# Kernel tuning notes

Hardware: AMD Instinct MI355X
Metric: run time of the kernel (lower is better)

## Reference

```python
import jax, jax.numpy as jnp
import numpy as np

D_MODEL = 2048
NUM_HEADS = 16
HEAD_DIM = D_MODEL // NUM_HEADS
B, T = 2, 2048


def setup_inputs() -> dict:
    key = jax.random.key(0)
    ks = jax.random.split(key, 6)
    x = jax.random.normal(ks[0], (B, T, D_MODEL), dtype=jnp.float32)
    # RoPE tables: angles theta_i = 10000^(-2i/d), half-dim tables [T, HEAD_DIM//2]
    pos = jnp.arange(T, dtype=jnp.float32)[:, None]
    inv_freq = 1.0 / (10000.0 ** (jnp.arange(0, HEAD_DIM, 2, dtype=jnp.float32) / HEAD_DIM))
    ang = pos * inv_freq[None, :]
    sin = jnp.sin(ang)
    cos = jnp.cos(ang)
    doc_ids = jnp.sort(jax.random.randint(ks[1], (B, T), 0, 4), axis=-1).astype(jnp.int32)
    W_qkv = jax.random.normal(ks[2], (D_MODEL, D_MODEL + 2 * HEAD_DIM), dtype=jnp.float32) * 0.02
    W_out = jax.random.normal(ks[3], (D_MODEL, D_MODEL), dtype=jnp.float32) * 0.02
    return {"x": x, "sin": sin, "cos": cos, "doc_ids": doc_ids, "W_qkv": W_qkv, "W_out": W_out}


def _apply_rope(x, sin, cos):
    # x: [..., T, ..., HEAD_DIM]; sin/cos: [T, HEAD_DIM//2], broadcast to x's rank
    if x.ndim == 4:  # [B, T, H, D]
        s, c = sin[None, :, None, :], cos[None, :, None, :]
    else:  # [B, T, D]
        s, c = sin[None, :, :], cos[None, :, :]
    x1, x2 = jnp.split(x, 2, axis=-1)
    return jnp.concatenate([x1 * c - x2 * s, x2 * c + x1 * s], axis=-1)


def reference(x, sin, cos, doc_ids, W_qkv, W_out):
    b, t, _ = x.shape
    qkv = x @ W_qkv  # [B, T, D_MODEL + 2*HEAD_DIM]
    q = qkv[..., :D_MODEL].reshape(b, t, NUM_HEADS, HEAD_DIM)
    k = qkv[..., D_MODEL:D_MODEL + HEAD_DIM]  # [B, T, HEAD_DIM] single KV head
    v = qkv[..., D_MODEL + HEAD_DIM:]         # [B, T, HEAD_DIM]
    q = _apply_rope(q, sin, cos)
    k = _apply_rope(k, sin, cos)
    # doc-packed causal mask -> additive bias [B, 1, T, T]
    neg_inf = jnp.finfo(q.dtype).min / 2
    causal = jnp.tril(jnp.ones((t, t), dtype=jnp.bool_))
    same_doc = doc_ids[:, :, None] == doc_ids[:, None, :]
    mask = (causal[None, :, :] & same_doc)[:, None, :, :]
    bias = jnp.where(mask, jnp.array(0.0, q.dtype), neg_inf)
    scale = 1.0 / jnp.sqrt(jnp.array(HEAD_DIM, q.dtype))
    scores = jnp.einsum("bthd,bsd->bhts", q, k) * scale + bias  # [B, H, T, T]
    attn = jax.nn.softmax(scores, axis=-1)
    out = jnp.einsum("bhts,bsd->bthd", attn, v).reshape(b, t, D_MODEL)
    return out @ W_out
```

## Files before the change

kernel.cpp:

```cpp
#include <hip/hip_runtime.h>
#include <math.h>

#define D_MODEL 2048
#define NUM_HEADS 16
#define HEAD_DIM 128
#define BB 2
#define TT 2048
#define QKV_N 2304
#define KOFF 2048
#define VOFF 2176

typedef __attribute__((ext_vector_type(8))) short short8;
typedef __attribute__((ext_vector_type(4))) float f32x4;

static __device__ __forceinline__ short f2bf(float f) {
  union { float f; unsigned u; } x; x.f = f;
  unsigned r = (x.u + 0x7FFFu + ((x.u >> 16) & 1u)) >> 16;
  return (short)r;
}

#define GLD16(gp, lp)                                              \
  __builtin_amdgcn_global_load_lds(                                \
      (const __attribute__((address_space(1))) void*)(gp),         \
      (__attribute__((address_space(3))) void*)(lp), 16, 0, 0)

static __device__ __forceinline__ void swizzle_xy(int& bx, int& by) {
  const int gx = gridDim.x;
  const int lin = blockIdx.y * gx + blockIdx.x;
  const int band = lin / (gx * 8);
  const int rem = lin - band * gx * 8;
  by = band * 8 + (rem & 7);
  bx = rem >> 3;
}

__global__ __launch_bounds__(256) void gemm_qkv_rope(
    const short* __restrict__ A, const short* __restrict__ Bt,
    short* __restrict__ qkv, short* __restrict__ Vtb,
    const float* __restrict__ sin_t, const float* __restrict__ cos_t)
{
  __shared__ short As[2 * 128 * 32];
  __shared__ short Bs[2 * 128 * 32];
  const int K = D_MODEL;

  int bx, by;
  swizzle_xy(bx, by);

  const int tid = threadIdx.x;
  const int w = tid >> 6, l = tid & 63;
  const int quad = l >> 4, l16 = l & 15;
  const int wm = w >> 1, wn = w & 1;
  const int m0 = by * 128, n0 = bx * 128;

  f32x4 acc[4][4];
#pragma unroll
  for (int i = 0; i < 4; i++)
#pragma unroll
    for (int j = 0; j < 4; j++) acc[i][j] = (f32x4){0.f, 0.f, 0.f, 0.f};

  const int cswz = ((l & 3) ^ ((l >> 3) & 3)) * 8;
  const short* aA = A + (size_t)(m0 + w * 32 + (l >> 2)) * K + cswz;
  const short* aB = Bt + (size_t)(n0 + w * 32 + (l >> 2)) * K + cswz;
  short* lA = As + w * 1024;
  short* lB = Bs + w * 1024;

  const int aswz = (quad ^ ((l16 >> 1) & 3)) * 8;
  const short* Ard = As + (size_t)(wm * 64 + l16) * 32 + aswz;
  const short* Brd = Bs + (size_t)(wn * 16 + l16) * 32 + aswz;

  for (int k0 = 0; k0 < K; k0 += 64) {
    __syncthreads();
#pragma unroll
    for (int h = 0; h < 2; h++) {
      const int go = k0 + h * 32;
      const int lo = h * 4096;
      GLD16(aA + go, lA + lo);
      GLD16(aA + go + (size_t)16 * K, lA + lo + 512);
      GLD16(aB + go, lB + lo);
      GLD16(aB + go + (size_t)16 * K, lB + lo + 512);
    }
    __syncthreads();

#pragma unroll
    for (int kc = 0; kc < 2; kc++) {
      short8 af[4], bf[4];
#pragma unroll
      for (int mi = 0; mi < 4; mi++)
        af[mi] = *(const short8*)(Ard + kc * 4096 + mi * 512);
#pragma unroll
      for (int ni = 0; ni < 4; ni++)
        bf[ni] = *(const short8*)(Brd + kc * 4096 + ni * 1024);
#pragma unroll
      for (int mi = 0; mi < 4; mi++)
#pragma unroll
        for (int ni = 0; ni < 4; ni++)
          acc[mi][ni] =
              __builtin_amdgcn_mfma_f32_16x16x32_bf16(af[mi], bf[ni], acc[mi][ni], 0, 0, 0);
    }
  }

  const int colbase = wn * 16 + l16;
  const bool is_v = (n0 == VOFF);

#pragma unroll
  for (int mi = 0; mi < 4; mi++) {
#pragma unroll
    for (int r = 0; r < 4; r++) {
      const int row = m0 + wm * 64 + mi * 16 + quad * 4 + r;
      const int b = row >> 11, t = row & (TT - 1);
#pragma unroll
      for (int ni = 0; ni < 2; ni++) {
        const int cloc = ni * 32 + colbase;
        const float c1 = acc[mi][ni][r];
        const float c2 = acc[mi][ni + 2][r];
        if (!is_v) {
          const float sn = sin_t[t * 64 + cloc];
          const float cs = cos_t[t * 64 + cloc];
          short* op = qkv + (size_t)row * QKV_N + n0 + cloc;
          op[0]  = f2bf(c1 * cs - c2 * sn);
          op[64] = f2bf(c2 * cs + c1 * sn);
        } else {
          Vtb[((size_t)(b * 128 + cloc) << 11) + t]      = f2bf(c1);
          Vtb[((size_t)(b * 128 + cloc + 64) << 11) + t] = f2bf(c2);
        }
      }
    }
  }
}

__global__ __launch_bounds__(256) void gemm_mfma_bt(
    const short* __restrict__ A, const short* __restrict__ Bt,
    float* __restrict__ C, int M, int N, int K)
{
  __shared__ short As[2 * 128 * 32];
  __shared__ short Bs[2 * 128 * 32];

  int bx, by;
  swizzle_xy(bx, by);

  const int tid = threadIdx.x;
  const int w = tid >> 6, l = tid & 63;
  const int quad = l >> 4, l16 = l & 15;
  const int wm = w >> 1, wn = w & 1;
  const int m0 = by * 128, n0 = bx * 128;

  f32x4 acc[4][4];
#pragma unroll
  for (int i = 0; i < 4; i++)
#pragma unroll
    for (int j = 0; j < 4; j++) acc[i][j] = (f32x4){0.f, 0.f, 0.f, 0.f};

  const int cswz = ((l & 3) ^ ((l >> 3) & 3)) * 8;
  const short* aA = A + (size_t)(m0 + w * 32 + (l >> 2)) * K + cswz;
  const short* aB = Bt + (size_t)(n0 + w * 32 + (l >> 2)) * K + cswz;
  short* lA = As + w * 1024;
  short* lB = Bs + w * 1024;

  const int aswz = (quad ^ ((l16 >> 1) & 3)) * 8;
  const short* Ard = As + (size_t)(wm * 64 + l16) * 32 + aswz;
  const short* Brd = Bs + (size_t)(wn * 64 + l16) * 32 + aswz;

  for (int k0 = 0; k0 < K; k0 += 64) {
    __syncthreads();
#pragma unroll
    for (int h = 0; h < 2; h++) {
      const int go = k0 + h * 32;
      const int lo = h * 4096;
      GLD16(aA + go, lA + lo);
      GLD16(aA + go + (size_t)16 * K, lA + lo + 512);
      GLD16(aB + go, lB + lo);
      GLD16(aB + go + (size_t)16 * K, lB + lo + 512);
    }
    __syncthreads();

#pragma unroll
    for (int kc = 0; kc < 2; kc++) {
      short8 af[4], bf[4];
#pragma unroll
      for (int mi = 0; mi < 4; mi++)
        af[mi] = *(const short8*)(Ard + kc * 4096 + mi * 512);
#pragma unroll
      for (int ni = 0; ni < 4; ni++)
        bf[ni] = *(const short8*)(Brd + kc * 4096 + ni * 512);
#pragma unroll
      for (int mi = 0; mi < 4; mi++)
#pragma unroll
        for (int ni = 0; ni < 4; ni++)
          acc[mi][ni] =
              __builtin_amdgcn_mfma_f32_16x16x32_bf16(af[mi], bf[ni], acc[mi][ni], 0, 0, 0);
    }
  }

#pragma unroll
  for (int mi = 0; mi < 4; mi++) {
#pragma unroll
    for (int ni = 0; ni < 4; ni++) {
#pragma unroll
      for (int r = 0; r < 4; r++) {
        const int row = m0 + wm * 64 + mi * 16 + quad * 4 + r;
        const int col = n0 + wn * 64 + ni * 16 + l16;
        C[(size_t)row * N + col] = acc[mi][ni][r];
      }
    }
  }
}

#define XC_BLOCKS 2048
#define WQT_TILES (36 * 32)
#define WOT_TILES (32 * 32)

__global__ __launch_bounds__(256) void prep_all(
    const float* __restrict__ x, short* __restrict__ xb,
    const float* __restrict__ Wq, short* __restrict__ Wqt,
    const float* __restrict__ Wo, short* __restrict__ Wot)
{
  const int bid = blockIdx.x;
  const int tid = threadIdx.x;

  if (bid < XC_BLOCKS) {
    const float4* xin = (const float4*)x;
    short4* xo = (short4*)xb;
    const size_t i0 = (size_t)bid * 256 + tid;
#pragma unroll
    for (int p = 0; p < 4; p++) {
      float4 v = xin[i0 + (size_t)p * 524288];
      short4 o;
      o.x = f2bf(v.x); o.y = f2bf(v.y); o.z = f2bf(v.z); o.w = f2bf(v.w);
      xo[i0 + (size_t)p * 524288] = o;
    }
    return;
  }

  __shared__ float t[64 * 64];
  int tile = bid - XC_BLOCKS;
  const float* W;
  short* Wt;
  int N, ntx;
  if (tile < WQT_TILES) {
    W = Wq; Wt = Wqt; N = QKV_N; ntx = 36;
  } else {
    tile -= WQT_TILES; W = Wo; Wt = Wot; N = D_MODEL; ntx = 32;
  }
  const int K = D_MODEL;
  const int n0 = (tile % ntx) * 64, k0 = (tile / ntx) * 64;

  {
    const int kl = tid >> 4;
    const int c4 = (tid & 15) * 4;
#pragma unroll
    for (int j = 0; j < 4; j++) {
      const int kr = kl + j * 16;
      float4 v = *(const float4*)(W + (size_t)(k0 + kr) * N + n0 + c4);
      *(float4*)(t + kr * 64 + (c4 ^ ((kr & 7) << 3))) = v;
    }
  }
  __syncthreads();
  {
    const int ks = (tid & 7) * 8;
#pragma unroll
    for (int j = 0; j < 2; j++) {
      const int nl = (tid >> 3) + j * 32;
      short8 o;
#pragma unroll
      for (int s = 0; s < 8; s++)
        o[s] = f2bf(t[(ks + s) * 64 + (nl ^ (s << 3))]);
      *(short8*)(Wt + (size_t)(n0 + nl) * K + k0 + ks) = o;
    }
  }
}

#define PSTR 72

__global__ __launch_bounds__(256, 2) void attn_mfma(
    const short* __restrict__ qkv, const short* __restrict__ Vtb,
    const int* __restrict__ doc_ids, short* __restrict__ attn_out)
{
  __shared__ short Ks[64 * 128];
  __shared__ short Vt[128 * 64];
  __shared__ short Pbuf[4 * 16 * PSTR];
  __shared__ int doc_s[64];

  const int h = blockIdx.y, b = blockIdx.z;
  const int qt0 = blockIdx.x;
  const int qt1 = 31 - qt0;
  const int tid = threadIdx.x;
  const int w = tid >> 6;
  const int lane = tid & 63;
  const int quad = lane >> 4, l16 = lane & 15;

  short8 Qf[2][4];
  int qg[2][4], mydoc[2][4];
  float l_i[2][4];
  f32x4 O[2][8];
  int docmin[2], docmax[2];

#pragma unroll
  for (int qi = 0; qi < 2; qi++) {
    const int q0 = (qi ? qt1 : qt0) * 64;
    const short* qp = qkv + (size_t)(b * TT + q0 + w * 16 + l16) * QKV_N
                      + h * HEAD_DIM + quad * 8;
#pragma unroll
    for (int kc = 0; kc < 4; kc++) Qf[qi][kc] = *(const short8*)(qp + kc * 32);
    docmin[qi] = doc_ids[b * TT + q0];
    docmax[qi] = doc_ids[b * TT + q0 + 63];
#pragma unroll
    for (int r = 0; r < 4; r++) {
      qg[qi][r] = q0 + w * 16 + quad * 4 + r;
      mydoc[qi][r] = doc_ids[b * TT + qg[qi][r]];
      l_i[qi][r] = 0.f;
    }
#pragma unroll
    for (int v8 = 0; v8 < 8; v8++) O[qi][v8] = (f32x4){0.f, 0.f, 0.f, 0.f};
  }

  short* Pw = Pbuf + w * 16 * PSTR;
  const float scale = 0.08838834764831844f;

  const int x7 = l16 & 7;
  int kcol[4], vcol[2];
#pragma unroll
  for (int kc = 0; kc < 4; kc++) kcol[kc] = ((kc * 4 + quad) ^ x7) * 8;
#pragma unroll
  for (int ks = 0; ks < 2; ks++) vcol[ks] = ((ks * 4 + quad) ^ x7) * 8;

  for (int st = 0; st <= qt1; st++) {
    const int s0 = st * 64;
    const int dmin_s = doc_ids[b * TT + s0];
    const int dmax_s = doc_ids[b * TT + s0 + 63];
    const bool act0 = (st <= qt0) && (dmax_s >= docmin[0]);
    const bool act1 = (dmax_s >= docmin[1]);
    if (!act0 && !act1) continue;
    const bool full0 = (st < qt0) && (dmin_s == docmax[0]);
    const bool full1 = (st < qt1) && (dmin_s == docmax[1]);
    const bool needdoc = (act0 && !full0) || (act1 && !full1);

    __syncthreads();
#pragma unroll
    for (int j = 0; j < 4; j++) {
      const int f = w * 4 + j;
      const int rg = f * 4 + (lane >> 4);
      GLD16(qkv + (size_t)(b * TT + s0 + rg) * QKV_N + KOFF
                + (((lane & 15) ^ (rg & 7)) * 8),
            Ks + f * 512);
    }
#pragma unroll
    for (int j = 0; j < 4; j++) {
      const int f = w * 4 + j;
      const int n = f * 8 + (lane >> 3);
      GLD16(Vtb + (((size_t)(b * 128 + n)) << 11) + s0
                + (((lane & 7) ^ (lane >> 3)) * 8),
            Vt + f * 512);
    }
    if (needdoc && tid < 64) doc_s[tid] = doc_ids[b * TT + s0 + tid];
    __syncthreads();

#pragma unroll
    for (int qi = 0; qi < 2; qi++) {
      const bool act = qi ? act1 : act0;
      if (!act) continue;
      const bool full = qi ? full1 : full0;

      f32x4 S[4];
#pragma unroll
      for (int ns = 0; ns < 4; ns++) {
        f32x4 acc = (f32x4){0.f, 0.f, 0.f, 0.f};
        const short* krow = Ks + (ns * 16 + l16) * 128;
#pragma unroll
        for (int kc = 0; kc < 4; kc++) {
          short8 kf = *(const short8*)(krow + kcol[kc]);
          acc = __builtin_amdgcn_mfma_f32_16x16x32_bf16(Qf[qi][kc], kf, acc, 0, 0, 0);
        }
        S[ns] = acc;
      }

      if (full) {
#pragma unroll
        for (int ns = 0; ns < 4; ns++)
#pragma unroll
          for (int r = 0; r < 4; r++) {
            const float p = __expf(S[ns][r] * scale);
            l_i[qi][r] += p;
            Pw[(quad * 4 + r) * PSTR + ns * 16 + l16] = f2bf(p);
          }
      } else {
#pragma unroll
        for (int ns = 0; ns < 4; ns++) {
          const int s_loc = ns * 16 + l16;
          const int sg = s0 + s_loc;
          const int sdoc = doc_s[s_loc];
#pragma unroll
          for (int r = 0; r < 4; r++) {
            const bool ok = (sg <= qg[qi][r]) && (sdoc == mydoc[qi][r]);
            const float p = ok ? __expf(S[ns][r] * scale) : 0.f;
            l_i[qi][r] += p;
            Pw[(quad * 4 + r) * PSTR + ns * 16 + l16] = f2bf(p);
          }
        }
      }

#pragma unroll
      for (int ks = 0; ks < 2; ks++) {
        short8 pf = *(const short8*)(Pw + l16 * PSTR + ks * 32 + quad * 8);
#pragma unroll
        for (int v8 = 0; v8 < 8; v8++) {
          short8 vf = *(const short8*)(Vt + (v8 * 16 + l16) * 64 + vcol[ks]);
          O[qi][v8] = __builtin_amdgcn_mfma_f32_16x16x32_bf16(pf, vf, O[qi][v8], 0, 0, 0);
        }
      }
    }
  }

#pragma unroll
  for (int qi = 0; qi < 2; qi++) {
#pragma unroll
    for (int off = 8; off >= 1; off >>= 1)
#pragma unroll
      for (int r = 0; r < 4; r++) l_i[qi][r] += __shfl_xor(l_i[qi][r], off);

#pragma unroll
    for (int r = 0; r < 4; r++) {
      const float inv = 1.f / l_i[qi][r];
      short* op = attn_out + (size_t)(b * TT + qg[qi][r]) * D_MODEL
                  + h * HEAD_DIM + l16;
#pragma unroll
      for (int v8 = 0; v8 < 8; v8++)
        op[v8 * 16] = f2bf(O[qi][v8][r] * inv);
    }
  }
}

extern "C" void kernel_launch(void* const* d_in, const int* in_sizes, int n_in,
                              void* d_out, int out_size, void* d_ws, size_t ws_size,
                              hipStream_t stream)
{
  const float* x     = (const float*)d_in[0];
  const float* sin_t = (const float*)d_in[1];
  const float* cos_t = (const float*)d_in[2];
  const int*   doc   = (const int*)  d_in[3];
  const float* W_qkv = (const float*)d_in[4];
  const float* W_out = (const float*)d_in[5];
  float* out = (float*)d_out;

  const int M = BB * TT;

  char* p = (char*)d_ws;
  short* qkv_bf = (short*)p; p += (size_t)M * QKV_N * 2;
  short* xb     = (short*)p; p += (size_t)M * D_MODEL * 2;
  short* attn_bf = xb;
  short* Vtb    = (short*)p; p += (size_t)BB * 128 * TT * 2;
  short* Wqkv_t = (short*)p; p += (size_t)QKV_N * D_MODEL * 2;
  short* Wout_t = (short*)p;

  prep_all<<<XC_BLOCKS + WQT_TILES + WOT_TILES, 256, 0, stream>>>(
      x, xb, W_qkv, Wqkv_t, W_out, Wout_t);

  {
    dim3 grid(QKV_N / 128, M / 128);
    gemm_qkv_rope<<<grid, 256, 0, stream>>>(xb, Wqkv_t, qkv_bf, Vtb, sin_t, cos_t);
  }
  {
    dim3 grid(TT / 128, NUM_HEADS, BB);
    attn_mfma<<<grid, 256, 0, stream>>>(qkv_bf, Vtb, doc, attn_bf);
  }
  {
    dim3 grid(D_MODEL / 128, M / 128);
    gemm_mfma_bt<<<grid, 256, 0, stream>>>(attn_bf, Wout_t, out, M, D_MODEL, D_MODEL);
  }
}
```

Baseline: 256.8 us.

## Double-buffer K/V tiles in attention and precompute active tile ranges

```diff
diff --git a/kernel.cpp b/kernel.cpp
--- a/kernel.cpp
+++ b/kernel.cpp
@@ -274,10 +274,10 @@
     const short* __restrict__ qkv, const short* __restrict__ Vtb,
     const int* __restrict__ doc_ids, short* __restrict__ attn_out)
 {
-  __shared__ short Ks[64 * 128];
-  __shared__ short Vt[128 * 64];
+  __shared__ short Ks[2][64 * 128];
+  __shared__ short Vt[2][128 * 64];
   __shared__ short Pbuf[4 * 16 * PSTR];
-  __shared__ int doc_s[64];
+  __shared__ int doc_s[2][64];
 
   const int h = blockIdx.y, b = blockIdx.z;
   const int qt0 = blockIdx.x;
@@ -312,6 +312,17 @@
     for (int v8 = 0; v8 < 8; v8++) O[qi][v8] = (f32x4){0.f, 0.f, 0.f, 0.f};
   }
 
+  int s0lo, s1lo;
+  {
+    const int st0 = lane < qt0 ? lane : qt0;
+    unsigned long long m0 = __ballot(doc_ids[b * TT + st0 * 64 + 63] >= docmin[0]);
+    s0lo = (int)__ffsll(m0) - 1;
+    const int st1 = lane < qt1 ? lane : qt1;
+    unsigned long long m1 = __ballot(doc_ids[b * TT + st1 * 64 + 63] >= docmin[1]);
+    s1lo = (int)__ffsll(m1) - 1;
+  }
+  const int s1b = (s1lo > qt0 + 1) ? s1lo : (qt0 + 1);
+
   short* Pw = Pbuf + w * 16 * PSTR;
   const float scale = 0.08838834764831844f;
 
@@ -322,36 +333,51 @@
 #pragma unroll
   for (int ks = 0; ks < 2; ks++) vcol[ks] = ((ks * 4 + quad) ^ x7) * 8;
 
-  for (int st = 0; st <= qt1; st++) {
-    const int s0 = st * 64;
-    const int dmin_s = doc_ids[b * TT + s0];
-    const int dmax_s = doc_ids[b * TT + s0 + 63];
-    const bool act0 = (st <= qt0) && (dmax_s >= docmin[0]);
-    const bool act1 = (dmax_s >= docmin[1]);
-    if (!act0 && !act1) continue;
-    const bool full0 = (st < qt0) && (dmin_s == docmax[0]);
-    const bool full1 = (st < qt1) && (dmin_s == docmax[1]);
-    const bool needdoc = (act0 && !full0) || (act1 && !full1);
-
-    __syncthreads();
+  auto stageKV = [&](int buf, int s0n) {
 #pragma unroll
     for (int j = 0; j < 4; j++) {
       const int f = w * 4 + j;
       const int rg = f * 4 + (lane >> 4);
-      GLD16(qkv + (size_t)(b * TT + s0 + rg) * QKV_N + KOFF
+      GLD16(qkv + (size_t)(b * TT + s0n + rg) * QKV_N + KOFF
                 + (((lane & 15) ^ (rg & 7)) * 8),
-            Ks + f * 512);
+            &Ks[buf][0] + f * 512);
     }
 #pragma unroll
     for (int j = 0; j < 4; j++) {
       const int f = w * 4 + j;
       const int n = f * 8 + (lane >> 3);
-      GLD16(Vtb + (((size_t)(b * 128 + n)) << 11) + s0
+      GLD16(Vtb + (((size_t)(b * 128 + n)) << 11) + s0n
                 + (((lane & 7) ^ (lane >> 3)) * 8),
-            Vt + f * 512);
-    }
-    if (needdoc && tid < 64) doc_s[tid] = doc_ids[b * TT + s0 + tid];
-    __syncthreads();
+            &Vt[buf][0] + f * 512);
+    }
+    if (tid < 64) doc_s[buf][tid] = doc_ids[b * TT + s0n + tid];
+  };
+
+  int st = s0lo, cur = 0;
+  stageKV(0, st * 64);
+
+  while (true) {
+    asm volatile("s_waitcnt lgkmcnt(0)" ::: "memory");
+    __builtin_amdgcn_s_barrier();
+    __builtin_amdgcn_sched_barrier(0);
+
+    const int nst = (st == qt1) ? -1 : (st == qt0 ? s1b : st + 1);
+    if (nst >= 0) stageKV(cur ^ 1, nst * 64);
+
+    if (nst >= 0) asm volatile("s_waitcnt vmcnt(8)" ::: "memory");
+    else          asm volatile("s_waitcnt vmcnt(0)" ::: "memory");
+    __builtin_amdgcn_s_barrier();
+    __builtin_amdgcn_sched_barrier(0);
+
+    const int s0 = st * 64;
+    const int dmin_s = doc_ids[b * TT + s0];
+    const bool act0 = (st <= qt0);
+    const bool act1 = (st >= s1lo);
+    const bool full0 = act0 && (st < qt0) && (dmin_s == docmax[0]);
+    const bool full1 = act1 && (st < qt1) && (dmin_s == docmax[1]);
+    const short* Kc = &Ks[cur][0];
+    const short* Vc = &Vt[cur][0];
+    const int* dc = doc_s[cur];
 
 #pragma unroll
     for (int qi = 0; qi < 2; qi++) {
@@ -363,7 +389,7 @@
 #pragma unroll
       for (int ns = 0; ns < 4; ns++) {
         f32x4 acc = (f32x4){0.f, 0.f, 0.f, 0.f};
-        const short* krow = Ks + (ns * 16 + l16) * 128;
+        const short* krow = Kc + (ns * 16 + l16) * 128;
 #pragma unroll
         for (int kc = 0; kc < 4; kc++) {
           short8 kf = *(const short8*)(krow + kcol[kc]);
@@ -386,7 +412,7 @@
         for (int ns = 0; ns < 4; ns++) {
           const int s_loc = ns * 16 + l16;
           const int sg = s0 + s_loc;
-          const int sdoc = doc_s[s_loc];
+          const int sdoc = dc[s_loc];
 #pragma unroll
           for (int r = 0; r < 4; r++) {
             const bool ok = (sg <= qg[qi][r]) && (sdoc == mydoc[qi][r]);
@@ -402,11 +428,15 @@
         short8 pf = *(const short8*)(Pw + l16 * PSTR + ks * 32 + quad * 8);
 #pragma unroll
         for (int v8 = 0; v8 < 8; v8++) {
-          short8 vf = *(const short8*)(Vt + (v8 * 16 + l16) * 64 + vcol[ks]);
+          short8 vf = *(const short8*)(Vc + (v8 * 16 + l16) * 64 + vcol[ks]);
           O[qi][v8] = __builtin_amdgcn_mfma_f32_16x16x32_bf16(pf, vf, O[qi][v8], 0, 0, 0);
         }
       }
     }
+
+    if (nst < 0) break;
+    st = nst;
+    cur ^= 1;
   }
 
 #pragma unroll
```

Result: no change. 257.4 us (+0.2%).
